# Kernel tuning notes

Measured on AMD Instinct MI355X. Metric: run time of the kernel, lower is better.

The kernel has to match this reference:

```python
import jax, jax.numpy as jnp
import numpy as np
from jax import lax

DIM = 64
BF = 2          # branching_factor
NUM_HEADS = 8
N_POS = 4096


def _expm(A, order=12, squarings=8):
    """Differentiable matrix exponential via scaling-and-squaring + Horner Taylor.
    Faithful substitute for torch.matrix_exp on skew-symmetric inputs."""
    d = A.shape[-1]
    I = jnp.eye(d, dtype=A.dtype)
    A = A / (2.0 ** squarings)
    E = I
    for k in range(order, 0, -1):
        E = I + jnp.matmul(A, E) / k
    for _ in range(squarings):
        E = jnp.matmul(E, E)
    return E


def _path_words_np(positions, bf):
    """Replicates create_paths + pad_sequence(padding_value=bf): tree path digits
    of node `pos` (root->leaf), right-padded with bf to the max actual length."""
    paths = []
    for p in positions:
        digs = []
        idx = int(p)
        while idx > 0:
            digs.append((idx - 1) % bf)
            idx = (idx - 1) // bf
        paths.append(digs[::-1] if p > 0 else [])
    T = max(1, max(len(p) for p in paths))
    out = np.full((len(paths), T), bf, dtype=np.int32)
    for i, p in enumerate(paths):
        out[i, :len(p)] = p
    return out


def setup_inputs() -> dict:
    key = jax.random.key(0)
    raw = jax.random.uniform(key, (BF * NUM_HEADS + 1, DIM, DIM), dtype=jnp.float32)
    # mimics torch.rand(...).softmax(-1).cumsum(-1) init of _primitives
    primitives_raw = jnp.cumsum(jax.nn.softmax(raw, axis=-1), axis=-1)
    positions = np.arange(N_POS)
    path_words = jnp.asarray(_path_words_np(positions, BF))  # [N, T] int32
    return {"primitives_raw": primitives_raw, "path_words": path_words}


def reference(primitives_raw, path_words):
    # primitives = matrix_exp(P - P^T)
    hermitian = primitives_raw - jnp.swapaxes(primitives_raw, -1, -2)
    primitives = _expm(hermitian)                      # [BF*H+1, d, d]
    d = primitives.shape[-1]
    I = jnp.eye(d, dtype=primitives.dtype)

    # linear(x, W) = x @ W.T; padding ids BF and BF+1 act as identity (no update)
    ext = jnp.concatenate(
        [jnp.swapaxes(primitives[:BF], -1, -2), jnp.broadcast_to(I, (2, d, d))],
        axis=0)                                        # [BF+2, d, d]

    n = path_words.shape[0]
    M0 = jnp.broadcast_to(I, (n, d, d))

    def body(M, w):  # w: [n] branch ids at this tree depth
        return jnp.einsum('nij,njk->nik', M, ext[w]), None

    M, _ = lax.scan(body, M0, path_words.T)            # fold over path depth
    maps = M[:, None]                                  # [n, 1, d, d]

    # create_steps: tree distance via common-prefix lengths
    pm = path_words != BF + 1                          # point mask [n, T]
    mask = pm[:, None, :] & pm[None, :, :]             # [n, n, T]
    eq = path_words[:, None, :] == path_words[None, :, :]
    common = lax.associative_scan(jnp.logical_and, eq, axis=-1) & mask
    lens = pm.sum(-1)
    steps = lens[:, None] + lens[None, :] - 2 * common.sum(-1).astype(lens.dtype)
    return maps, steps
```

## Files before the change

### kernel.cpp

```cpp
#include <hip/hip_runtime.h>


#define NPOS 4096
#define TLEN 12

typedef __attribute__((ext_vector_type(8))) short short8;
typedef __attribute__((ext_vector_type(4))) float f32x4;
typedef __attribute__((ext_vector_type(2))) float f32x2;

__device__ __forceinline__ unsigned short f2bf(float f) {
  union { float f; unsigned u; } v; v.f = f;
  unsigned r = v.u + 0x7fffu + ((v.u >> 16) & 1u);
  return (unsigned short)(r >> 16);
}

__device__ __forceinline__ void mm64p(const float (*P)[68], const float (*B)[68],
                                      f32x2 acc[4][2], int r0, int c0) {
#pragma unroll 4
  for (int k0 = 0; k0 < 64; k0 += 4) {
    float a[4][4];
#pragma unroll
    for (int i = 0; i < 4; ++i) {
      const float4 t4 = *reinterpret_cast<const float4*>(&P[r0 + i][k0]);
      a[i][0] = t4.x; a[i][1] = t4.y; a[i][2] = t4.z; a[i][3] = t4.w;
    }
#pragma unroll
    for (int kk = 0; kk < 4; ++kk) {
      const float4 bv = *reinterpret_cast<const float4*>(&B[k0 + kk][c0]);
      const f32x2 lo = {bv.x, bv.y}, hi = {bv.z, bv.w};
#pragma unroll
      for (int i = 0; i < 4; ++i) {
        acc[i][0] += a[i][kk] * lo;
        acc[i][1] += a[i][kk] * hi;
      }
    }
  }
}

__device__ __forceinline__ float step_val(unsigned a, unsigned b) {
  const unsigned x = a ^ b;
  const int cp = x ? (__builtin_clz(x) >> 1) : TLEN;
  return (float)(2 * TLEN - 2 * cp);
}

__global__ __launch_bounds__(256) void expm_steps_kernel(
    const float* __restrict__ raw, const unsigned* __restrict__ keys,
    unsigned short* __restrict__ tabR, unsigned short* __restrict__ tabT,
    float* __restrict__ steps_out) {
  __shared__ float P[64][68];
  __shared__ float Bs[64][68];
  const int t = threadIdx.x;

  if (blockIdx.x >= 2) {
    const int b = (int)blockIdx.x - 2;
    const int i = b >> 2;
    const int j0 = ((b & 3) << 10) | (t << 2);
    const unsigned ki = keys[i];
    const uint4 kj = *reinterpret_cast<const uint4*>(&keys[j0]);
    float4 r;
    r.x = step_val(ki, kj.x);
    r.y = step_val(ki, kj.y);
    r.z = step_val(ki, kj.z);
    r.w = step_val(ki, kj.w);
    *reinterpret_cast<float4*>(&steps_out[(size_t)i * NPOS + j0]) = r;
    return;
  }

  const int d = blockIdx.x;
  const int r0 = (t >> 4) << 2, c0 = (t & 15) << 2;
  const float* R = raw + d * 4096;
  float a_[4][4], a2_[4][4], e_[4][4];
  f32x2 acc[4][2];
#define ZACC { _Pragma("unroll") for (int i = 0; i < 4; ++i) { acc[i][0] = f32x2{0.f,0.f}; acc[i][1] = f32x2{0.f,0.f}; } }
#define GETACC(i, j) ((j) < 2 ? acc[i][0][j] : acc[i][1][(j)-2])

#pragma unroll
  for (int i = 0; i < 4; ++i)
#pragma unroll
    for (int j = 0; j < 4; ++j)
      a_[i][j] = (R[(r0 + i) * 64 + c0 + j] - R[(c0 + j) * 64 + r0 + i]) * (1.0f / 64.0f);
#pragma unroll
  for (int i = 0; i < 4; ++i) {
    const float4 v = make_float4(a_[i][0], a_[i][1], a_[i][2], a_[i][3]);
    *reinterpret_cast<float4*>(&P[r0 + i][c0]) = v;
    *reinterpret_cast<float4*>(&Bs[r0 + i][c0]) = v;
  }
  __syncthreads();

  ZACC; mm64p(P, Bs, acc, r0, c0);
  __syncthreads();
#pragma unroll
  for (int i = 0; i < 4; ++i) {
#pragma unroll
    for (int j = 0; j < 4; ++j) a2_[i][j] = GETACC(i, j);
    *reinterpret_cast<float4*>(&Bs[r0 + i][c0]) =
        make_float4(a2_[i][0], a2_[i][1], a2_[i][2], a2_[i][3]);
  }
  __syncthreads();

  ZACC; mm64p(P, Bs, acc, r0, c0);
  __syncthreads();
#pragma unroll
  for (int i = 0; i < 4; ++i) {
    float q[4];
#pragma unroll
    for (int j = 0; j < 4; ++j) {
      const float id = (r0 + i == c0 + j) ? 1.0f : 0.0f;
      q[j] = (1.0f / 362880.0f) * id + (1.0f / 3628800.0f) * a_[i][j] +
             (1.0f / 39916800.0f) * a2_[i][j];
    }
    *reinterpret_cast<float4*>(&Bs[r0 + i][c0]) =
        make_float4(GETACC(i, 0), GETACC(i, 1), GETACC(i, 2), GETACC(i, 3));
    *reinterpret_cast<float4*>(&P[r0 + i][c0]) = make_float4(q[0], q[1], q[2], q[3]);
  }
  __syncthreads();

  const float C[3][3] = {{1.0f / 720.0f, 1.0f / 5040.0f, 1.0f / 40320.0f},
                         {1.0f / 6.0f, 1.0f / 24.0f, 1.0f / 120.0f},
                         {1.0f, 1.0f, 0.5f}};
#pragma unroll
  for (int h = 0; h < 3; ++h) {
    ZACC; mm64p(P, Bs, acc, r0, c0);
    __syncthreads();
#pragma unroll
    for (int i = 0; i < 4; ++i) {
      float q[4];
#pragma unroll
      for (int j = 0; j < 4; ++j) {
        const float id = (r0 + i == c0 + j) ? 1.0f : 0.0f;
        q[j] = GETACC(i, j) + C[h][0] * id + C[h][1] * a_[i][j] + C[h][2] * a2_[i][j];
      }
      const float4 v = make_float4(q[0], q[1], q[2], q[3]);
      *reinterpret_cast<float4*>(&P[r0 + i][c0]) = v;
      if (h == 2) *reinterpret_cast<float4*>(&Bs[r0 + i][c0]) = v;
    }
    __syncthreads();
  }

  for (int s = 0; s < 6; ++s) {
    ZACC; mm64p(P, Bs, acc, r0, c0);
    __syncthreads();
#pragma unroll
    for (int i = 0; i < 4; ++i)
#pragma unroll
      for (int j = 0; j < 4; ++j) e_[i][j] = GETACC(i, j);
    if (s < 5) {
#pragma unroll
      for (int i = 0; i < 4; ++i) {
        const float4 v = make_float4(e_[i][0], e_[i][1], e_[i][2], e_[i][3]);
        *reinterpret_cast<float4*>(&P[r0 + i][c0]) = v;
        *reinterpret_cast<float4*>(&Bs[r0 + i][c0]) = v;
      }
      __syncthreads();
    }
  }

  unsigned short* oR = tabR + (size_t)(1 + d) * 4096;
  unsigned short* oT = tabT + (size_t)(1 + d) * 4096;
#pragma unroll
  for (int i = 0; i < 4; ++i)
#pragma unroll
    for (int j = 0; j < 4; ++j) {
      const unsigned short v = f2bf(e_[i][j]);
      oR[(c0 + j) * 64 + (r0 + i)] = v;
      oT[(r0 + i) * 64 + (c0 + j)] = v;
    }
  if (d == 0) {
#pragma unroll
    for (int i = 0; i < 16; ++i) {
      const int idx = (i << 8) | t;
      const int r = idx >> 6, c = idx & 63;
      const unsigned short v = (r == c) ? (unsigned short)0x3F80 : (unsigned short)0;
      tabR[idx] = v;
      tabT[idx] = v;
    }
  }
#undef ZACC
#undef GETACC
}

__device__ __forceinline__ void mfma64(const unsigned short* __restrict__ X,
                                       const unsigned short* __restrict__ Yt,
                                       f32x4 acc[4], int wv, int l) {
  const int row = l & 15, g = l >> 4;
  short8 a[2], b[4][2];
#pragma unroll
  for (int q = 0; q < 2; ++q)
    a[q] = *reinterpret_cast<const short8*>(X + (((16 * wv + row) << 6) | (q << 5) | (g << 3)));
#pragma unroll
  for (int c = 0; c < 4; ++c)
#pragma unroll
    for (int q = 0; q < 2; ++q)
      b[c][q] = *reinterpret_cast<const short8*>(Yt + (((16 * c + row) << 6) | (q << 5) | (g << 3)));
#pragma unroll
  for (int c = 0; c < 4; ++c) {
    acc[c] = __builtin_amdgcn_mfma_f32_16x16x32_bf16(a[0], b[c][0], acc[c], 0, 0, 0);
    acc[c] = __builtin_amdgcn_mfma_f32_16x16x32_bf16(a[1], b[c][1], acc[c], 0, 0, 0);
  }
}

__global__ __launch_bounds__(256) void pairs_kernel(unsigned short* __restrict__ tabR,
                                                    unsigned short* __restrict__ tabT) {
  __shared__ unsigned short Tl[64][72];
  const int e = 3 + (int)blockIdx.x;
  const int lev = 31 - __clz(e + 1);
  const int v = (e + 1) - (1 << lev);
  const int wv = threadIdx.x >> 6, l = threadIdx.x & 63;
  const int row = l & 15, g = l >> 4;

  short8 bT[2][4][2];
#pragma unroll
  for (int dd = 0; dd < 2; ++dd)
#pragma unroll
    for (int c = 0; c < 4; ++c)
#pragma unroll
      for (int q = 0; q < 2; ++q)
        bT[dd][c][q] = *reinterpret_cast<const short8*>(
            tabT + (size_t)(1 + dd) * 4096 + (((16 * c + row) << 6) | (q << 5) | (g << 3)));

  const int d0 = (v >> (lev - 1)) & 1;
  short8 a[2];
#pragma unroll
  for (int q = 0; q < 2; ++q)
    a[q] = *reinterpret_cast<const short8*>(
        tabR + (size_t)(1 + d0) * 4096 + (((16 * wv + row) << 6) | (q << 5) | (g << 3)));

  f32x4 acc[4] = {f32x4{0,0,0,0}, f32x4{0,0,0,0}, f32x4{0,0,0,0}, f32x4{0,0,0,0}};
  const int d1 = (v >> (lev - 2)) & 1;
#pragma unroll
  for (int c = 0; c < 4; ++c) {
    acc[c] = __builtin_amdgcn_mfma_f32_16x16x32_bf16(a[0], bT[d1][c][0], acc[c], 0, 0, 0);
    acc[c] = __builtin_amdgcn_mfma_f32_16x16x32_bf16(a[1], bT[d1][c][1], acc[c], 0, 0, 0);
  }

  for (int j = 2; j < lev; ++j) {
    const int dj = (v >> (lev - 1 - j)) & 1;
#pragma unroll
    for (int c = 0; c < 4; ++c)
#pragma unroll
      for (int r = 0; r < 4; ++r)
        Tl[16 * wv + 4 * g + r][16 * c + row] = f2bf(acc[c][r]);
    __syncthreads();
#pragma unroll
    for (int q = 0; q < 2; ++q)
      a[q] = *reinterpret_cast<const short8*>(&Tl[16 * wv + row][(q << 5) | (g << 3)]);
    __syncthreads();
#pragma unroll
    for (int c = 0; c < 4; ++c) {
      acc[c] = f32x4{0, 0, 0, 0};
      acc[c] = __builtin_amdgcn_mfma_f32_16x16x32_bf16(a[0], bT[dj][c][0], acc[c], 0, 0, 0);
      acc[c] = __builtin_amdgcn_mfma_f32_16x16x32_bf16(a[1], bT[dj][c][1], acc[c], 0, 0, 0);
    }
  }

  unsigned short* oR = tabR + (size_t)e * 4096;
  unsigned short* oT = tabT + (size_t)e * 4096;
#pragma unroll
  for (int c = 0; c < 4; ++c)
#pragma unroll
    for (int r = 0; r < 4; ++r) {
      const unsigned short val = f2bf(acc[c][r]);
      const int rr = 16 * wv + 4 * g + r, cc = 16 * c + row;
      oR[rr * 64 + cc] = val;
      oT[cc * 64 + rr] = val;
    }
}

__global__ __launch_bounds__(256) void maps_kernel(const int* __restrict__ pw,
                                                   const unsigned short* __restrict__ tabR,
                                                   const unsigned short* __restrict__ tabT,
                                                   float* __restrict__ out) {
  __shared__ float T[64][68];
  const int n = blockIdx.x;
  const int t = threadIdx.x;
  int v1 = 0, l1 = 0, v2 = 0, l2 = 0;
#pragma unroll
  for (int tt = 0; tt < 6; ++tt) {
    const int w = pw[n * TLEN + tt];
    if (w < 2) { v1 = (v1 << 1) | w; ++l1; }
  }
#pragma unroll
  for (int tt = 6; tt < 12; ++tt) {
    const int w = pw[n * TLEN + tt];
    if (w < 2) { v2 = (v2 << 1) | w; ++l2; }
  }
  const int wv = t >> 6, l = t & 63;
  f32x4 acc[4] = {f32x4{0,0,0,0}, f32x4{0,0,0,0}, f32x4{0,0,0,0}, f32x4{0,0,0,0}};
  mfma64(tabR + (size_t)((1 << l1) - 1 + v1) * 4096,
         tabT + (size_t)((1 << l2) - 1 + v2) * 4096, acc, wv, l);
  const int row = l & 15, g = l >> 4;
#pragma unroll
  for (int c = 0; c < 4; ++c)
#pragma unroll
    for (int r = 0; r < 4; ++r)
      T[16 * wv + 4 * g + r][16 * c + row] = acc[c][r];
  __syncthreads();
  float* O = out + (size_t)n * 4096;
#pragma unroll
  for (int p = 0; p < 4; ++p) {
    const int idx = (p << 8) | t;
    const int rr = idx >> 4, cc = (idx & 15) << 2;
    *reinterpret_cast<float4*>(&O[(rr << 6) | cc]) =
        *reinterpret_cast<const float4*>(&T[rr][cc]);
  }
}

__global__ __launch_bounds__(256) void keys_kernel(const int* __restrict__ pw,
                                                   unsigned* __restrict__ keys) {
  const int n = blockIdx.x * 256 + threadIdx.x;
  unsigned k = 0;
#pragma unroll
  for (int tt = 0; tt < TLEN; ++tt) k = (k << 2) | (unsigned)pw[n * TLEN + tt];
  keys[n] = k << 8;
}

extern "C" void kernel_launch(void* const* d_in, const int* in_sizes, int n_in,
                              void* d_out, int out_size, void* d_ws, size_t ws_size,
                              hipStream_t stream) {
  const float* raw = (const float*)d_in[0];
  const int* pw = (const int*)d_in[1];
  float* out = (float*)d_out;

  unsigned short* tabR = (unsigned short*)d_ws;
  unsigned short* tabT = tabR + (size_t)127 * 4096;
  unsigned* keys = (unsigned*)((char*)d_ws + (4u << 20));

  keys_kernel<<<NPOS / 256, 256, 0, stream>>>(pw, keys);
  expm_steps_kernel<<<2 + NPOS * 4, 256, 0, stream>>>(raw, keys, tabR, tabT,
                                                      out + (size_t)NPOS * 4096);
  pairs_kernel<<<124, 256, 0, stream>>>(tabR, tabT);
  maps_kernel<<<NPOS, 256, 0, stream>>>(pw, tabR, tabT, out);
}
```

Baseline: 199.1 us.

## Compute matrix exponential with split-bf16 MFMA instead of scalar fp32 FMA

Replaces the scalar fp32 shared-memory 64x64 matmuls in the expm stage with bf16 MFMA instructions. Each operand is split into high and low bf16 parts and multiplied with three MFMAs to keep near-fp32 accuracy. Skew-symmetry is exploited: transposes are obtained by sign flips of fragments, and E and E^T are carried together through the squarings. This removes the long serial FMA chain in the two expm blocks, which likely dominate latency alongside the steps blocks. In exchange it accepts some precision risk and uses more shared memory and registers.

```diff
diff --git a/kernel.cpp b/kernel.cpp
--- a/kernel.cpp
+++ b/kernel.cpp
@@ -3,39 +3,48 @@
 
 #define NPOS 4096
 #define TLEN 12
+#define LDB 72
 
 typedef __attribute__((ext_vector_type(8))) short short8;
 typedef __attribute__((ext_vector_type(4))) float f32x4;
-typedef __attribute__((ext_vector_type(2))) float f32x2;
+typedef __attribute__((ext_vector_type(4))) unsigned short us4;
 
 __device__ __forceinline__ unsigned short f2bf(float f) {
   union { float f; unsigned u; } v; v.f = f;
   unsigned r = v.u + 0x7fffu + ((v.u >> 16) & 1u);
   return (unsigned short)(r >> 16);
 }
-
-__device__ __forceinline__ void mm64p(const float (*P)[68], const float (*B)[68],
-                                      f32x2 acc[4][2], int r0, int c0) {
-#pragma unroll 4
-  for (int k0 = 0; k0 < 64; k0 += 4) {
-    float a[4][4];
-#pragma unroll
-    for (int i = 0; i < 4; ++i) {
-      const float4 t4 = *reinterpret_cast<const float4*>(&P[r0 + i][k0]);
-      a[i][0] = t4.x; a[i][1] = t4.y; a[i][2] = t4.z; a[i][3] = t4.w;
-    }
-#pragma unroll
-    for (int kk = 0; kk < 4; ++kk) {
-      const float4 bv = *reinterpret_cast<const float4*>(&B[k0 + kk][c0]);
-      const f32x2 lo = {bv.x, bv.y}, hi = {bv.z, bv.w};
-#pragma unroll
-      for (int i = 0; i < 4; ++i) {
-        acc[i][0] += a[i][kk] * lo;
-        acc[i][1] += a[i][kk] * hi;
-      }
-    }
-  }
-}
+__device__ __forceinline__ float bf2f(unsigned short h) {
+  union { unsigned u; float f; } v; v.u = ((unsigned)h) << 16;
+  return v.f;
+}
+__device__ __forceinline__ short8 flip8(short8 x) {
+  union { short8 s; uint4 u; } v; v.s = x;
+  v.u.x ^= 0x80008000u; v.u.y ^= 0x80008000u;
+  v.u.z ^= 0x80008000u; v.u.w ^= 0x80008000u;
+  return v.s;
+}
+__device__ __forceinline__ short8 ldfrag(const short* T, int ridx, int q, int g) {
+  return *reinterpret_cast<const short8*>(&T[ridx * LDB + (q << 5) + (g << 3)]);
+}
+__device__ __forceinline__ void wsplit4(short* Th, short* Tl, int ridx, int col0,
+                                        float v0, float v1, float v2, float v3) {
+  us4 H, L;
+  const float vv[4] = {v0, v1, v2, v3};
+#pragma unroll
+  for (int j = 0; j < 4; ++j) {
+    const unsigned short h = f2bf(vv[j]);
+    H[j] = h;
+    L[j] = f2bf(vv[j] - bf2f(h));
+  }
+  *reinterpret_cast<us4*>(&Th[ridx * LDB + col0]) = H;
+  *reinterpret_cast<us4*>(&Tl[ridx * LDB + col0]) = L;
+}
+
+#define MFMA3(ACC, AH, AL, BH, BL)                                          \
+  ACC = __builtin_amdgcn_mfma_f32_16x16x32_bf16(AH, BH, ACC, 0, 0, 0);      \
+  ACC = __builtin_amdgcn_mfma_f32_16x16x32_bf16(AH, BL, ACC, 0, 0, 0);      \
+  ACC = __builtin_amdgcn_mfma_f32_16x16x32_bf16(AL, BH, ACC, 0, 0, 0);
 
 __device__ __forceinline__ float step_val(unsigned a, unsigned b) {
   const unsigned x = a ^ b;
@@ -43,12 +52,11 @@
   return (float)(2 * TLEN - 2 * cp);
 }
 
-__global__ __launch_bounds__(256) void expm_steps_kernel(
+__global__ __launch_bounds__(256, 1) void expm_steps_kernel(
     const float* __restrict__ raw, const unsigned* __restrict__ keys,
     unsigned short* __restrict__ tabR, unsigned short* __restrict__ tabT,
     float* __restrict__ steps_out) {
-  __shared__ float P[64][68];
-  __shared__ float Bs[64][68];
+  __shared__ short bufS[6][64 * LDB];
   const int t = threadIdx.x;
 
   if (blockIdx.x >= 2) {
@@ -66,90 +74,212 @@
     return;
   }
 
+  short* A_h = bufS[0];  short* A_l = bufS[1];
+  short* Q_h = bufS[2];  short* Q_l = bufS[3];
+  short* A3_h = bufS[4]; short* A3_l = bufS[5];
+  short* Et_h = bufS[0]; short* Et_l = bufS[1];
+  float* F = reinterpret_cast<float*>(bufS[4]);
+
   const int d = blockIdx.x;
-  const int r0 = (t >> 4) << 2, c0 = (t & 15) << 2;
-  const float* R = raw + d * 4096;
-  float a_[4][4], a2_[4][4], e_[4][4];
-  f32x2 acc[4][2];
-#define ZACC { _Pragma("unroll") for (int i = 0; i < 4; ++i) { acc[i][0] = f32x2{0.f,0.f}; acc[i][1] = f32x2{0.f,0.f}; } }
-#define GETACC(i, j) ((j) < 2 ? acc[i][0][j] : acc[i][1][(j)-2])
-
-#pragma unroll
-  for (int i = 0; i < 4; ++i)
-#pragma unroll
-    for (int j = 0; j < 4; ++j)
-      a_[i][j] = (R[(r0 + i) * 64 + c0 + j] - R[(c0 + j) * 64 + r0 + i]) * (1.0f / 64.0f);
-#pragma unroll
-  for (int i = 0; i < 4; ++i) {
-    const float4 v = make_float4(a_[i][0], a_[i][1], a_[i][2], a_[i][3]);
-    *reinterpret_cast<float4*>(&P[r0 + i][c0]) = v;
-    *reinterpret_cast<float4*>(&Bs[r0 + i][c0]) = v;
-  }
-  __syncthreads();
-
-  ZACC; mm64p(P, Bs, acc, r0, c0);
-  __syncthreads();
-#pragma unroll
-  for (int i = 0; i < 4; ++i) {
-#pragma unroll
-    for (int j = 0; j < 4; ++j) a2_[i][j] = GETACC(i, j);
-    *reinterpret_cast<float4*>(&Bs[r0 + i][c0]) =
-        make_float4(a2_[i][0], a2_[i][1], a2_[i][2], a2_[i][3]);
-  }
-  __syncthreads();
-
-  ZACC; mm64p(P, Bs, acc, r0, c0);
-  __syncthreads();
-#pragma unroll
-  for (int i = 0; i < 4; ++i) {
-    float q[4];
-#pragma unroll
-    for (int j = 0; j < 4; ++j) {
-      const float id = (r0 + i == c0 + j) ? 1.0f : 0.0f;
-      q[j] = (1.0f / 362880.0f) * id + (1.0f / 3628800.0f) * a_[i][j] +
-             (1.0f / 39916800.0f) * a2_[i][j];
-    }
-    *reinterpret_cast<float4*>(&Bs[r0 + i][c0]) =
-        make_float4(GETACC(i, 0), GETACC(i, 1), GETACC(i, 2), GETACC(i, 3));
-    *reinterpret_cast<float4*>(&P[r0 + i][c0]) = make_float4(q[0], q[1], q[2], q[3]);
-  }
-  __syncthreads();
-
-  const float C[3][3] = {{1.0f / 720.0f, 1.0f / 5040.0f, 1.0f / 40320.0f},
-                         {1.0f / 6.0f, 1.0f / 24.0f, 1.0f / 120.0f},
-                         {1.0f, 1.0f, 0.5f}};
-#pragma unroll
-  for (int h = 0; h < 3; ++h) {
-    ZACC; mm64p(P, Bs, acc, r0, c0);
-    __syncthreads();
-#pragma unroll
-    for (int i = 0; i < 4; ++i) {
-      float q[4];
-#pragma unroll
-      for (int j = 0; j < 4; ++j) {
-        const float id = (r0 + i == c0 + j) ? 1.0f : 0.0f;
-        q[j] = GETACC(i, j) + C[h][0] * id + C[h][1] * a_[i][j] + C[h][2] * a2_[i][j];
-      }
-      const float4 v = make_float4(q[0], q[1], q[2], q[3]);
-      *reinterpret_cast<float4*>(&P[r0 + i][c0]) = v;
-      if (h == 2) *reinterpret_cast<float4*>(&Bs[r0 + i][c0]) = v;
+  const int wv = t >> 6, l = t & 63;
+  const int row = l & 15, g = l >> 4;
+
+#pragma unroll
+  for (int i = 0; i < 16; ++i) F[(i << 8) | t] = raw[d * 4096 + ((i << 8) | t)];
+  __syncthreads();
+
+  {
+    const int r = t & 63, cs = (t >> 6) << 4;
+#pragma unroll
+    for (int j4 = 0; j4 < 4; ++j4) {
+      const int c = cs + (j4 << 2);
+      float v[4];
+#pragma unroll
+      for (int j = 0; j < 4; ++j)
+        v[j] = (F[(r << 6) + c + j] - F[((c + j) << 6) + r]) * (1.0f / 64.0f);
+      wsplit4(A_h, A_l, r, c, v[0], v[1], v[2], v[3]);
+    }
+  }
+  float a_c[4][4], a2_c[4][4];
+#pragma unroll
+  for (int c = 0; c < 4; ++c)
+#pragma unroll
+    for (int r = 0; r < 4; ++r) {
+      const int RR = 16 * wv + 4 * g + r, CC = 16 * c + row;
+      a_c[c][r] = (F[(RR << 6) + CC] - F[(CC << 6) + RR]) * (1.0f / 64.0f);
+    }
+  __syncthreads();
+
+  f32x4 acc1[4], acc2[4];
+
+#pragma unroll
+  for (int c = 0; c < 4; ++c) acc1[c] = f32x4{0, 0, 0, 0};
+  {
+    short8 aH[2], aL[2];
+#pragma unroll
+    for (int q = 0; q < 2; ++q) {
+      aH[q] = ldfrag(A_h, 16 * wv + row, q, g);
+      aL[q] = ldfrag(A_l, 16 * wv + row, q, g);
+    }
+#pragma unroll
+    for (int c = 0; c < 4; ++c)
+#pragma unroll
+      for (int q = 0; q < 2; ++q) {
+        const short8 bh = flip8(ldfrag(A_h, 16 * c + row, q, g));
+        const short8 bl = flip8(ldfrag(A_l, 16 * c + row, q, g));
+        MFMA3(acc1[c], aH[q], aL[q], bh, bl);
+      }
+  }
+#pragma unroll
+  for (int c = 0; c < 4; ++c) {
+#pragma unroll
+    for (int r = 0; r < 4; ++r) a2_c[c][r] = acc1[c][r];
+    wsplit4(Q_h, Q_l, 16 * c + row, 16 * wv + 4 * g,
+            acc1[c][0], acc1[c][1], acc1[c][2], acc1[c][3]);
+  }
+  __syncthreads();
+
+#pragma unroll
+  for (int c = 0; c < 4; ++c) acc1[c] = f32x4{0, 0, 0, 0};
+  {
+    short8 aH[2], aL[2];
+#pragma unroll
+    for (int q = 0; q < 2; ++q) {
+      aH[q] = ldfrag(Q_h, 16 * wv + row, q, g);
+      aL[q] = ldfrag(Q_l, 16 * wv + row, q, g);
+    }
+#pragma unroll
+    for (int c = 0; c < 4; ++c)
+#pragma unroll
+      for (int q = 0; q < 2; ++q) {
+        const short8 bh = flip8(ldfrag(A_h, 16 * c + row, q, g));
+        const short8 bl = flip8(ldfrag(A_l, 16 * c + row, q, g));
+        MFMA3(acc1[c], aH[q], aL[q], bh, bl);
+      }
+  }
+#pragma unroll
+  for (int c = 0; c < 4; ++c)
+    wsplit4(A3_h, A3_l, 16 * c + row, 16 * wv + 4 * g,
+            -acc1[c][0], -acc1[c][1], -acc1[c][2], -acc1[c][3]);
+  __syncthreads();
+
+#pragma unroll
+  for (int c = 0; c < 4; ++c) {
+    float v[4];
+#pragma unroll
+    for (int r = 0; r < 4; ++r) {
+      const float id = ((16 * wv + 4 * g + r) == (16 * c + row)) ? 1.0f : 0.0f;
+      v[r] = (1.0f / 362880.0f) * id - (1.0f / 3628800.0f) * a_c[c][r] +
+             (1.0f / 39916800.0f) * a2_c[c][r];
+    }
+    wsplit4(Q_h, Q_l, 16 * c + row, 16 * wv + 4 * g, v[0], v[1], v[2], v[3]);
+  }
+  __syncthreads();
+
+  const float CH[3][3] = {{1.f / 720.f, 1.f / 5040.f, 1.f / 40320.f},
+                          {1.f / 6.f, 1.f / 24.f, 1.f / 120.f},
+                          {1.f, 1.f, 0.5f}};
+
+#pragma unroll
+  for (int h = 0; h < 2; ++h) {
+    short8 qH[4][2], qL[4][2], a3H[2], a3L[2];
+#pragma unroll
+    for (int c = 0; c < 4; ++c)
+#pragma unroll
+      for (int q = 0; q < 2; ++q) {
+        qH[c][q] = ldfrag(Q_h, 16 * c + row, q, g);
+        qL[c][q] = ldfrag(Q_l, 16 * c + row, q, g);
+      }
+#pragma unroll
+    for (int q = 0; q < 2; ++q) {
+      a3H[q] = ldfrag(A3_h, 16 * wv + row, q, g);
+      a3L[q] = ldfrag(A3_l, 16 * wv + row, q, g);
+    }
+    __syncthreads();
+#pragma unroll
+    for (int c = 0; c < 4; ++c) acc2[c] = f32x4{0, 0, 0, 0};
+#pragma unroll
+    for (int c = 0; c < 4; ++c)
+#pragma unroll
+      for (int q = 0; q < 2; ++q) { MFMA3(acc2[c], a3H[q], a3L[q], qH[c][q], qL[c][q]); }
+#pragma unroll
+    for (int c = 0; c < 4; ++c) {
+      float v[4];
+#pragma unroll
+      for (int r = 0; r < 4; ++r) {
+        const float id = ((16 * wv + 4 * g + r) == (16 * c + row)) ? 1.0f : 0.0f;
+        v[r] = -acc2[c][r] + CH[h][0] * id - CH[h][1] * a_c[c][r] + CH[h][2] * a2_c[c][r];
+      }
+      wsplit4(Q_h, Q_l, 16 * c + row, 16 * wv + 4 * g, v[0], v[1], v[2], v[3]);
+    }
+    __syncthreads();
+  }
+
+  {
+    short8 qH[4][2], qL[4][2], t3H[4][2], t3L[4][2];
+#pragma unroll
+    for (int c = 0; c < 4; ++c)
+#pragma unroll
+      for (int q = 0; q < 2; ++q) {
+        qH[c][q] = ldfrag(Q_h, 16 * c + row, q, g);
+        qL[c][q] = ldfrag(Q_l, 16 * c + row, q, g);
+        t3H[c][q] = flip8(ldfrag(A3_h, 16 * c + row, q, g));
+        t3L[c][q] = flip8(ldfrag(A3_l, 16 * c + row, q, g));
+      }
+    __syncthreads();
+#pragma unroll
+    for (int c = 0; c < 4; ++c) { acc1[c] = f32x4{0, 0, 0, 0}; acc2[c] = f32x4{0, 0, 0, 0}; }
+#pragma unroll
+    for (int c = 0; c < 4; ++c)
+#pragma unroll
+      for (int q = 0; q < 2; ++q) {
+        MFMA3(acc1[c], qH[wv][q], qL[wv][q], t3H[c][q], t3L[c][q]);
+        const short8 aH = flip8(t3H[wv][q]), aL = flip8(t3L[wv][q]);
+        MFMA3(acc2[c], aH, aL, qH[c][q], qL[c][q]);
+      }
+#pragma unroll
+    for (int c = 0; c < 4; ++c) {
+      float v1[4], v2[4];
+#pragma unroll
+      for (int r = 0; r < 4; ++r) {
+        const float id = ((16 * wv + 4 * g + r) == (16 * c + row)) ? 1.0f : 0.0f;
+        v1[r] = acc1[c][r] + CH[2][0] * id + CH[2][1] * a_c[c][r] + CH[2][2] * a2_c[c][r];
+        v2[r] = -acc2[c][r] + CH[2][0] * id - CH[2][1] * a_c[c][r] + CH[2][2] * a2_c[c][r];
+      }
+      wsplit4(Et_h, Et_l, 16 * c + row, 16 * wv + 4 * g, v1[0], v1[1], v1[2], v1[3]);
+      wsplit4(Q_h, Q_l, 16 * c + row, 16 * wv + 4 * g, v2[0], v2[1], v2[2], v2[3]);
     }
     __syncthreads();
   }
 
   for (int s = 0; s < 6; ++s) {
-    ZACC; mm64p(P, Bs, acc, r0, c0);
-    __syncthreads();
-#pragma unroll
-    for (int i = 0; i < 4; ++i)
-#pragma unroll
-      for (int j = 0; j < 4; ++j) e_[i][j] = GETACC(i, j);
+    short8 eH[4][2], eL[4][2], tH[4][2], tL[4][2];
+#pragma unroll
+    for (int c = 0; c < 4; ++c)
+#pragma unroll
+      for (int q = 0; q < 2; ++q) {
+        eH[c][q] = ldfrag(Q_h, 16 * c + row, q, g);
+        eL[c][q] = ldfrag(Q_l, 16 * c + row, q, g);
+        tH[c][q] = ldfrag(Et_h, 16 * c + row, q, g);
+        tL[c][q] = ldfrag(Et_l, 16 * c + row, q, g);
+      }
+    __syncthreads();
+#pragma unroll
+    for (int c = 0; c < 4; ++c) { acc1[c] = f32x4{0, 0, 0, 0}; acc2[c] = f32x4{0, 0, 0, 0}; }
+#pragma unroll
+    for (int c = 0; c < 4; ++c)
+#pragma unroll
+      for (int q = 0; q < 2; ++q) {
+        MFMA3(acc1[c], eH[wv][q], eL[wv][q], tH[c][q], tL[c][q]);
+        MFMA3(acc2[c], tH[wv][q], tL[wv][q], eH[c][q], eL[c][q]);
+      }
     if (s < 5) {
 #pragma unroll
-      for (int i = 0; i < 4; ++i) {
-        const float4 v = make_float4(e_[i][0], e_[i][1], e_[i][2], e_[i][3]);
-        *reinterpret_cast<float4*>(&P[r0 + i][c0]) = v;
-        *reinterpret_cast<float4*>(&Bs[r0 + i][c0]) = v;
+      for (int c = 0; c < 4; ++c) {
+        wsplit4(Et_h, Et_l, 16 * c + row, 16 * wv + 4 * g,
+                acc1[c][0], acc1[c][1], acc1[c][2], acc1[c][3]);
+        wsplit4(Q_h, Q_l, 16 * c + row, 16 * wv + 4 * g,
+                acc2[c][0], acc2[c][1], acc2[c][2], acc2[c][3]);
       }
       __syncthreads();
     }
@@ -158,12 +288,13 @@
   unsigned short* oR = tabR + (size_t)(1 + d) * 4096;
   unsigned short* oT = tabT + (size_t)(1 + d) * 4096;
 #pragma unroll
-  for (int i = 0; i < 4; ++i)
-#pragma unroll
-    for (int j = 0; j < 4; ++j) {
-      const unsigned short v = f2bf(e_[i][j]);
-      oR[(c0 + j) * 64 + (r0 + i)] = v;
-      oT[(r0 + i) * 64 + (c0 + j)] = v;
+  for (int c = 0; c < 4; ++c)
+#pragma unroll
+    for (int r = 0; r < 4; ++r) {
+      const int RR = 16 * wv + 4 * g + r, CC = 16 * c + row;
+      const unsigned short vbf = f2bf(acc1[c][r]);
+      oR[CC * 64 + RR] = vbf;
+      oT[RR * 64 + CC] = vbf;
     }
   if (d == 0) {
 #pragma unroll
@@ -175,8 +306,6 @@
       tabT[idx] = v;
     }
   }
-#undef ZACC
-#undef GETACC
 }
 
 __device__ __forceinline__ void mfma64(const unsigned short* __restrict__ X,
```

Measured after the change: 428.3 us. 2.15x slower.
